# Kernel optimization log

Hardware: AMD Instinct MI355X
Metric: run time of the kernel (lower is better)

## Reference

```python
import jax, jax.numpy as jnp
import numpy as np

N = 50000
E = 1_600_000
IN_C, HID_C, OUT_C = 128, 64, 16
NEG_SLOPE = 0.2


def setup_inputs() -> dict:
    key = jax.random.key(0)
    ks = jax.random.split(key, 16)
    x = jax.random.normal(ks[0], (N, IN_C), dtype=jnp.float32)
    edge_index = jax.random.randint(ks[1], (2, E), 0, N, dtype=jnp.int32)
    edge_weight = jax.random.uniform(ks[2], (E,), dtype=jnp.float32)

    def lin(k, fan_in, fan_out):
        s = (6.0 / (fan_in + fan_out)) ** 0.5
        return jax.random.uniform(k, (fan_in, fan_out), jnp.float32, -s, s)

    params = {
        "W1": lin(ks[3], IN_C, HID_C),
        "a_src1": jax.random.normal(ks[4], (HID_C,), jnp.float32) * 0.1,
        "a_dst1": jax.random.normal(ks[5], (HID_C,), jnp.float32) * 0.1,
        "b1": jnp.zeros((HID_C,), jnp.float32),
        "W2": lin(ks[6], HID_C, HID_C),
        "a_src2": jax.random.normal(ks[7], (HID_C,), jnp.float32) * 0.1,
        "a_dst2": jax.random.normal(ks[8], (HID_C,), jnp.float32) * 0.1,
        "b2": jnp.zeros((HID_C,), jnp.float32),
        "W3": lin(ks[9], HID_C, OUT_C),
        "a_src3": jax.random.normal(ks[10], (OUT_C,), jnp.float32) * 0.1,
        "a_dst3": jax.random.normal(ks[11], (OUT_C,), jnp.float32) * 0.1,
        "b3": jnp.zeros((OUT_C,), jnp.float32),
    }
    return {"x": x, "edge_index": edge_index, "edge_weight": edge_weight, **params}


def gat_conv(x, W, a_src, a_dst, b, src, dst):
    """Single-head PyG GATConv, add_self_loops=False, eval mode."""
    h = x @ W                                    # [N, C]
    alpha_src = (h * a_src).sum(-1)              # [N]
    alpha_dst = (h * a_dst).sum(-1)              # [N]
    e = jax.nn.leaky_relu(alpha_src[src] + alpha_dst[dst], NEG_SLOPE)  # [E]
    # softmax over incoming edges of each target node
    m = jax.ops.segment_max(e, dst, num_segments=N)
    e = jnp.exp(e - m[dst])
    denom = jax.ops.segment_sum(e, dst, num_segments=N)
    alpha = e / (denom[dst] + 1e-16)             # [E]
    out = jax.ops.segment_sum(h[src] * alpha[:, None], dst, num_segments=N)
    return out + b


def reference(x, edge_index, edge_weight,
              W1, a_src1, a_dst1, b1,
              W2, a_src2, a_dst2, b2,
              W3, a_src3, a_dst3, b3):
    src, dst = edge_index[0], edge_index[1]
    # edge_weight unused: GATConv has no lin_edge (edge_dim=None)
    h = jax.nn.relu(gat_conv(x, W1, a_src1, a_dst1, b1, src, dst))
    h = jax.nn.relu(gat_conv(h, W2, a_src2, a_dst2, b2, src, dst))
    return gat_conv(h, W3, a_src3, a_dst3, b3, src, dst)
```

## Files before the change

### kernel.cpp

```cpp
#include <hip/hip_runtime.h>
#include <hip/hip_fp16.h>
#include <math.h>

#define N_NODES 50000
#define N_EDGES 1600000
#define BSH 8
#define NBUCK ((N_NODES + 255) >> BSH)
#define EPB 4096
#define NBLK ((N_EDGES + EPB - 1) / EPB)


__global__ __launch_bounds__(256) void bucket_hist(const int* __restrict__ dst,
                                                   int* __restrict__ bhist_t, int e) {
    __shared__ int h[NBUCK];
    for (int i = threadIdx.x; i < NBUCK; i += 256) h[i] = 0;
    __syncthreads();
    int base = blockIdx.x * EPB;
#pragma unroll
    for (int j = 0; j < EPB / 256; ++j) {
        int i = base + j * 256 + threadIdx.x;
        if (i < e) atomicAdd(&h[dst[i] >> BSH], 1);
    }
    __syncthreads();
    for (int i = threadIdx.x; i < NBUCK; i += 256)
        bhist_t[i * NBLK + blockIdx.x] = h[i];
}

__global__ __launch_bounds__(256) void bucket_totals(const int* __restrict__ bhist_t,
                                                     int* __restrict__ btot) {
    int b = blockIdx.x;
    const int* col = bhist_t + (size_t)b * NBLK;
    int s = 0;
    for (int i = threadIdx.x; i < NBLK; i += 256) s += col[i];
#pragma unroll
    for (int off = 1; off < 64; off <<= 1) s += __shfl_xor(s, off);
    __shared__ int red[4];
    if ((threadIdx.x & 63) == 0) red[threadIdx.x >> 6] = s;
    __syncthreads();
    if (threadIdx.x == 0)
        btot[b] = red[0] + red[1] + red[2] + red[3];
}

__global__ __launch_bounds__(64) void rewrite_offsets(int* __restrict__ bhist_t,
                                                      const int* __restrict__ btot,
                                                      int* __restrict__ rowptr) {
    int b = blockIdx.x;
    int lane = threadIdx.x;
    int pre = 0;
    for (int i = lane; i < NBUCK; i += 64) if (i < b) pre += btot[i];
#pragma unroll
    for (int off = 1; off < 64; off <<= 1) pre += __shfl_xor(pre, off);
    if (b == 0 && lane == 0) rowptr[N_NODES] = N_EDGES;

    int* col = bhist_t + (size_t)b * NBLK;
    __shared__ int buf[NBLK];
    for (int i = lane; i < NBLK; i += 64) buf[i] = col[i];
    __syncthreads();
    constexpr int CH = (NBLK + 63) / 64;
    int lo = lane * CH;
    int hi = lo + CH; if (hi > NBLK) hi = NBLK;
    int s = 0;
    for (int i = lo; i < hi; ++i) s += buf[i];
    int inc = s;
#pragma unroll
    for (int off = 1; off < 64; off <<= 1) {
        int t = __shfl_up(inc, off);
        if (lane >= off) inc += t;
    }
    int run = pre + inc - s;
    for (int i = lo; i < hi; ++i) { int c = buf[i]; col[i] = run; run += c; }
}

__global__ __launch_bounds__(256) void bucket_scatter(const int* __restrict__ src,
                                                      const int* __restrict__ dst,
                                                      const int* __restrict__ bhist_t,
                                                      unsigned* __restrict__ packed, int e) {
    __shared__ int lcur[NBUCK];
    int r = blockIdx.x;
    for (int i = threadIdx.x; i < NBUCK; i += 256)
        lcur[i] = bhist_t[i * NBLK + r];
    __syncthreads();
    int base = r * EPB;
#pragma unroll
    for (int j = 0; j < EPB / 256; ++j) {
        int i = base + j * 256 + threadIdx.x;
        if (i < e) {
            int d = dst[i];
            int pos = atomicAdd(&lcur[d >> BSH], 1);
            packed[pos] = (unsigned)src[i] | ((unsigned)(d & ((1 << BSH) - 1)) << 16);
        }
    }
}

__global__ __launch_bounds__(512) void csr_finalize(const unsigned* __restrict__ packed,
                                                    const int* __restrict__ btot,
                                                    int* __restrict__ rowptr,
                                                    int* __restrict__ csr_src) {
    int b = blockIdx.x;
    __shared__ int sb[2];
    if (threadIdx.x < 64) {
        int pre = 0, tot = 0;
        for (int i = threadIdx.x; i < NBUCK; i += 64) {
            int v = btot[i];
            if (i < b) pre += v;
            if (i == b) tot = v;
        }
#pragma unroll
        for (int off = 1; off < 64; off <<= 1) {
            pre += __shfl_xor(pre, off);
            tot += __shfl_xor(tot, off);
        }
        if (threadIdx.x == 0) { sb[0] = pre; sb[1] = pre + tot; }
    }
    __syncthreads();
    int s0 = sb[0], s1 = sb[1];
    int cnt = s1 - s0;
    __shared__ int ncnt[256];
    __shared__ int ncur[256];
    __shared__ int wsum[4];
    if (threadIdx.x < 256) ncnt[threadIdx.x] = 0;
    __syncthreads();
    for (int i = threadIdx.x; i < cnt; i += 512)
        atomicAdd(&ncnt[packed[s0 + i] >> 16], 1);
    __syncthreads();
    int lane = threadIdx.x & 63, w = threadIdx.x >> 6;
    int v = 0, inc = 0;
    if (threadIdx.x < 256) {
        v = ncnt[threadIdx.x]; inc = v;
#pragma unroll
        for (int off = 1; off < 64; off <<= 1) {
            int t = __shfl_up(inc, off);
            if (lane >= off) inc += t;
        }
        if (lane == 63) wsum[w] = inc;
    }
    __syncthreads();
    if (threadIdx.x < 256) {
        int woff = 0;
#pragma unroll
        for (int k = 0; k < 3; ++k) if (k < w) woff += wsum[k];
        int excl = woff + inc - v;
        int node = (b << BSH) + threadIdx.x;
        if (node < N_NODES) rowptr[node] = s0 + excl;
        ncur[threadIdx.x] = s0 + excl;
    }
    __syncthreads();
    for (int i = threadIdx.x; i < cnt; i += 512) {
        unsigned p = packed[s0 + i];
        int pos = atomicAdd(&ncur[p >> 16], 1);
        csr_src[pos] = (int)(p & 0xFFFFu);
    }
}


template<int K, int C, bool IN_HALF, bool OUT_HALF>
__global__ __launch_bounds__(256) void gemm_alpha(
        const void* __restrict__ inv, const float* __restrict__ W,
        const float* __restrict__ a_src, const float* __restrict__ a_dst,
        void* __restrict__ hv, float* __restrict__ as_, float* __restrict__ ad_, int n)
{
    constexpr int CPT = C / 16;
    constexpr int KP = K + 4;
    __shared__ float sx[64][KP];
    __shared__ float sW[K * C];
    int row0 = blockIdx.x * 64;
    int nvalid = n - row0;

    if constexpr (IN_HALF) {
        const __half* inh = (const __half*)inv;
        for (int idx = threadIdx.x; idx < 64 * K / 8; idx += 256) {
            int r = idx / (K / 8), kc = idx % (K / 8);
            uint4 v = {0u, 0u, 0u, 0u};
            if (r < nvalid) v = *(const uint4*)&inh[(size_t)(row0 + r) * K + kc * 8];
            float2 f0 = __half22float2(*(__half2*)&v.x);
            float2 f1 = __half22float2(*(__half2*)&v.y);
            float2 f2 = __half22float2(*(__half2*)&v.z);
            float2 f3 = __half22float2(*(__half2*)&v.w);
            float* d = &sx[r][kc * 8];
            d[0] = f0.x; d[1] = f0.y; d[2] = f1.x; d[3] = f1.y;
            d[4] = f2.x; d[5] = f2.y; d[6] = f3.x; d[7] = f3.y;
        }
    } else {
        const float* in = (const float*)inv;
        for (int idx = threadIdx.x; idx < 64 * K / 4; idx += 256) {
            int r = idx / (K / 4), kc = idx % (K / 4);
            float4 v = {0, 0, 0, 0};
            if (r < nvalid) v = *(const float4*)&in[(size_t)(row0 + r) * K + kc * 4];
            *(float4*)&sx[r][kc * 4] = v;
        }
    }
    for (int idx = threadIdx.x; idx < K * C / 4; idx += 256)
        *(float4*)&sW[idx * 4] = *(const float4*)&W[idx * 4];
    __syncthreads();

    int g  = threadIdx.x >> 4;
    int ci = threadIdx.x & 15;
    int r0 = g * 4;
    int c0 = ci * CPT;

    if constexpr (CPT == 4) {
        float4 acc0 = {0,0,0,0}, acc1 = {0,0,0,0}, acc2 = {0,0,0,0}, acc3 = {0,0,0,0};
        for (int k = 0; k < K; k += 4) {
            float4 w0 = *(const float4*)&sW[(k + 0) * C + c0];
            float4 w1 = *(const float4*)&sW[(k + 1) * C + c0];
            float4 w2 = *(const float4*)&sW[(k + 2) * C + c0];
            float4 w3 = *(const float4*)&sW[(k + 3) * C + c0];
            float4 x0 = *(const float4*)&sx[r0 + 0][k];
            float4 x1 = *(const float4*)&sx[r0 + 1][k];
            float4 x2 = *(const float4*)&sx[r0 + 2][k];
            float4 x3 = *(const float4*)&sx[r0 + 3][k];
#define STEP(A, X) \
            A.x = fmaf(X.x, w0.x, A.x); A.y = fmaf(X.x, w0.y, A.y); \
            A.z = fmaf(X.x, w0.z, A.z); A.w = fmaf(X.x, w0.w, A.w); \
            A.x = fmaf(X.y, w1.x, A.x); A.y = fmaf(X.y, w1.y, A.y); \
            A.z = fmaf(X.y, w1.z, A.z); A.w = fmaf(X.y, w1.w, A.w); \
            A.x = fmaf(X.z, w2.x, A.x); A.y = fmaf(X.z, w2.y, A.y); \
            A.z = fmaf(X.z, w2.z, A.z); A.w = fmaf(X.z, w2.w, A.w); \
            A.x = fmaf(X.w, w3.x, A.x); A.y = fmaf(X.w, w3.y, A.y); \
            A.z = fmaf(X.w, w3.z, A.z); A.w = fmaf(X.w, w3.w, A.w);
            STEP(acc0, x0) STEP(acc1, x1) STEP(acc2, x2) STEP(acc3, x3)
#undef STEP
        }
        if constexpr (OUT_HALF) {
            __half* hh = (__half*)hv;
            auto sth = [&](int r, float4 a) {
                if (r0 + r < nvalid) {
                    size_t base = (size_t)(row0 + r0 + r) * C + c0;
                    *(__half2*)&hh[base]     = __floats2half2_rn(a.x, a.y);
                    *(__half2*)&hh[base + 2] = __floats2half2_rn(a.z, a.w);
                }
            };
            sth(0, acc0); sth(1, acc1); sth(2, acc2); sth(3, acc3);
        } else {
            float* h = (float*)hv;
            if (r0 + 0 < nvalid) *(float4*)&h[(size_t)(row0 + r0 + 0) * C + c0] = acc0;
            if (r0 + 1 < nvalid) *(float4*)&h[(size_t)(row0 + r0 + 1) * C + c0] = acc1;
            if (r0 + 2 < nvalid) *(float4*)&h[(size_t)(row0 + r0 + 2) * C + c0] = acc2;
            if (r0 + 3 < nvalid) *(float4*)&h[(size_t)(row0 + r0 + 3) * C + c0] = acc3;
        }
        float4 asv = *(const float4*)&a_src[c0];
        float4 adv = *(const float4*)&a_dst[c0];
        float vs0 = acc0.x*asv.x + acc0.y*asv.y + acc0.z*asv.z + acc0.w*asv.w;
        float vs1 = acc1.x*asv.x + acc1.y*asv.y + acc1.z*asv.z + acc1.w*asv.w;
        float vs2 = acc2.x*asv.x + acc2.y*asv.y + acc2.z*asv.z + acc2.w*asv.w;
        float vs3 = acc3.x*asv.x + acc3.y*asv.y + acc3.z*asv.z + acc3.w*asv.w;
        float vd0 = acc0.x*adv.x + acc0.y*adv.y + acc0.z*adv.z + acc0.w*adv.w;
        float vd1 = acc1.x*adv.x + acc1.y*adv.y + acc1.z*adv.z + acc1.w*adv.w;
        float vd2 = acc2.x*adv.x + acc2.y*adv.y + acc2.z*adv.z + acc2.w*adv.w;
        float vd3 = acc3.x*adv.x + acc3.y*adv.y + acc3.z*adv.z + acc3.w*adv.w;
#pragma unroll
        for (int off = 1; off < 16; off <<= 1) {
            vs0 += __shfl_xor(vs0, off); vs1 += __shfl_xor(vs1, off);
            vs2 += __shfl_xor(vs2, off); vs3 += __shfl_xor(vs3, off);
            vd0 += __shfl_xor(vd0, off); vd1 += __shfl_xor(vd1, off);
            vd2 += __shfl_xor(vd2, off); vd3 += __shfl_xor(vd3, off);
        }
        if (ci == 0) {
            if (r0 + 0 < nvalid) { as_[row0+r0+0] = vs0; ad_[row0+r0+0] = vd0; }
            if (r0 + 1 < nvalid) { as_[row0+r0+1] = vs1; ad_[row0+r0+1] = vd1; }
            if (r0 + 2 < nvalid) { as_[row0+r0+2] = vs2; ad_[row0+r0+2] = vd2; }
            if (r0 + 3 < nvalid) { as_[row0+r0+3] = vs3; ad_[row0+r0+3] = vd3; }
        }
    } else {
        float s0 = 0.f, s1 = 0.f, s2 = 0.f, s3 = 0.f;
        for (int k = 0; k < K; k += 4) {
            float w0 = sW[(k + 0) * C + c0];
            float w1 = sW[(k + 1) * C + c0];
            float w2 = sW[(k + 2) * C + c0];
            float w3 = sW[(k + 3) * C + c0];
            float4 x0 = *(const float4*)&sx[r0 + 0][k];
            float4 x1 = *(const float4*)&sx[r0 + 1][k];
            float4 x2 = *(const float4*)&sx[r0 + 2][k];
            float4 x3 = *(const float4*)&sx[r0 + 3][k];
            s0 = fmaf(x0.x,w0, fmaf(x0.y,w1, fmaf(x0.z,w2, fmaf(x0.w,w3, s0))));
            s1 = fmaf(x1.x,w0, fmaf(x1.y,w1, fmaf(x1.z,w2, fmaf(x1.w,w3, s1))));
            s2 = fmaf(x2.x,w0, fmaf(x2.y,w1, fmaf(x2.z,w2, fmaf(x2.w,w3, s2))));
            s3 = fmaf(x3.x,w0, fmaf(x3.y,w1, fmaf(x3.z,w2, fmaf(x3.w,w3, s3))));
        }
        if constexpr (OUT_HALF) {
            __half* hh = (__half*)hv;
            if (r0 + 0 < nvalid) hh[(size_t)(row0+r0+0) * C + c0] = __float2half_rn(s0);
            if (r0 + 1 < nvalid) hh[(size_t)(row0+r0+1) * C + c0] = __float2half_rn(s1);
            if (r0 + 2 < nvalid) hh[(size_t)(row0+r0+2) * C + c0] = __float2half_rn(s2);
            if (r0 + 3 < nvalid) hh[(size_t)(row0+r0+3) * C + c0] = __float2half_rn(s3);
        } else {
            float* h = (float*)hv;
            if (r0 + 0 < nvalid) h[(size_t)(row0+r0+0) * C + c0] = s0;
            if (r0 + 1 < nvalid) h[(size_t)(row0+r0+1) * C + c0] = s1;
            if (r0 + 2 < nvalid) h[(size_t)(row0+r0+2) * C + c0] = s2;
            if (r0 + 3 < nvalid) h[(size_t)(row0+r0+3) * C + c0] = s3;
        }
        float as0 = a_src[c0], ad0 = a_dst[c0];
        float vs0 = s0*as0, vs1 = s1*as0, vs2 = s2*as0, vs3 = s3*as0;
        float vd0 = s0*ad0, vd1 = s1*ad0, vd2 = s2*ad0, vd3 = s3*ad0;
#pragma unroll
        for (int off = 1; off < 16; off <<= 1) {
            vs0 += __shfl_xor(vs0, off); vs1 += __shfl_xor(vs1, off);
            vs2 += __shfl_xor(vs2, off); vs3 += __shfl_xor(vs3, off);
            vd0 += __shfl_xor(vd0, off); vd1 += __shfl_xor(vd1, off);
            vd2 += __shfl_xor(vd2, off); vd3 += __shfl_xor(vd3, off);
        }
        if (ci == 0) {
            if (r0 + 0 < nvalid) { as_[row0+r0+0] = vs0; ad_[row0+r0+0] = vd0; }
            if (r0 + 1 < nvalid) { as_[row0+r0+1] = vs1; ad_[row0+r0+1] = vd1; }
            if (r0 + 2 < nvalid) { as_[row0+r0+2] = vs2; ad_[row0+r0+2] = vd2; }
            if (r0 + 3 < nvalid) { as_[row0+r0+3] = vs3; ad_[row0+r0+3] = vd3; }
        }
    }
}


__device__ __forceinline__ float leaky(float e) {
    return (e >= 0.f) ? e : 0.2f * e;
}

__device__ __forceinline__ void hacc8(uint4 r, float w, float4& accL, float4& accH) {
    float2 f0 = __half22float2(*(__half2*)&r.x);
    float2 f1 = __half22float2(*(__half2*)&r.y);
    float2 f2 = __half22float2(*(__half2*)&r.z);
    float2 f3 = __half22float2(*(__half2*)&r.w);
    accL.x = fmaf(w, f0.x, accL.x); accL.y = fmaf(w, f0.y, accL.y);
    accL.z = fmaf(w, f1.x, accL.z); accL.w = fmaf(w, f1.y, accL.w);
    accH.x = fmaf(w, f2.x, accH.x); accH.y = fmaf(w, f2.y, accH.y);
    accH.z = fmaf(w, f3.x, accH.z); accH.w = fmaf(w, f3.y, accH.w);
}

template<bool RELU>
__global__ __launch_bounds__(256) void agg64h(
        const __half* __restrict__ h, const float* __restrict__ as_, const float* __restrict__ ad_,
        const int* __restrict__ rowptr, const int* __restrict__ csr_src,
        const float* __restrict__ bias, __half* __restrict__ out, int n)
{
    int node = (blockIdx.x * blockDim.x + threadIdx.x) >> 6;
    if (node >= n) return;
    int lane = threadIdx.x & 63;
    int g  = lane >> 3;
    int c8 = lane & 7;
    int start = rowptr[node], end = rowptr[node + 1];
    float adn = ad_[node];
    const char* hb = (const char*)h + (size_t)c8 * 16;

    float4 accL = {0,0,0,0}, accH = {0,0,0,0};
    float dsum = 0.f;

    for (int chunk = start; chunk < end; chunk += 64) {
        int e_i = chunk + lane;
        int soff = 0; float aw = 0.f;
        if (e_i < end) {
            int ssrc = csr_src[e_i];
            soff = ssrc << 7;
            aw = __expf(leaky(as_[ssrc] + adn));
        }
        dsum += aw;
        int nv = end - chunk; if (nv > 64) nv = 64;
        int nvu = (nv + 31) & ~31;
        for (int j = g; j < nvu; j += 32) {
            int   o0 = __shfl(soff, j),      o1 = __shfl(soff, j + 8);
            int   o2 = __shfl(soff, j + 16), o3 = __shfl(soff, j + 24);
            float w0 = __shfl(aw, j),        w1 = __shfl(aw, j + 8);
            float w2 = __shfl(aw, j + 16),   w3 = __shfl(aw, j + 24);
            uint4 r0 = *(const uint4*)(hb + o0);
            uint4 r1 = *(const uint4*)(hb + o1);
            uint4 r2 = *(const uint4*)(hb + o2);
            uint4 r3 = *(const uint4*)(hb + o3);
            hacc8(r0, w0, accL, accH); hacc8(r1, w1, accL, accH);
            hacc8(r2, w2, accL, accH); hacc8(r3, w3, accL, accH);
        }
    }
#pragma unroll
    for (int off = 8; off <= 32; off <<= 1) {
        accL.x += __shfl_xor(accL.x, off); accL.y += __shfl_xor(accL.y, off);
        accL.z += __shfl_xor(accL.z, off); accL.w += __shfl_xor(accL.w, off);
        accH.x += __shfl_xor(accH.x, off); accH.y += __shfl_xor(accH.y, off);
        accH.z += __shfl_xor(accH.z, off); accH.w += __shfl_xor(accH.w, off);
    }
#pragma unroll
    for (int off = 1; off <= 32; off <<= 1) dsum += __shfl_xor(dsum, off);

    if (g == 0) {
        float inv = 1.f / (dsum + 1e-16f);
        float4 bl = *(const float4*)&bias[c8 * 8];
        float4 bh = *(const float4*)&bias[c8 * 8 + 4];
        float4 ol, oh;
        ol.x = fmaf(accL.x, inv, bl.x); ol.y = fmaf(accL.y, inv, bl.y);
        ol.z = fmaf(accL.z, inv, bl.z); ol.w = fmaf(accL.w, inv, bl.w);
        oh.x = fmaf(accH.x, inv, bh.x); oh.y = fmaf(accH.y, inv, bh.y);
        oh.z = fmaf(accH.z, inv, bh.z); oh.w = fmaf(accH.w, inv, bh.w);
        if (RELU) {
            ol.x = fmaxf(ol.x, 0.f); ol.y = fmaxf(ol.y, 0.f);
            ol.z = fmaxf(ol.z, 0.f); ol.w = fmaxf(ol.w, 0.f);
            oh.x = fmaxf(oh.x, 0.f); oh.y = fmaxf(oh.y, 0.f);
            oh.z = fmaxf(oh.z, 0.f); oh.w = fmaxf(oh.w, 0.f);
        }
        __half2 p0 = __floats2half2_rn(ol.x, ol.y);
        __half2 p1 = __floats2half2_rn(ol.z, ol.w);
        __half2 p2 = __floats2half2_rn(oh.x, oh.y);
        __half2 p3 = __floats2half2_rn(oh.z, oh.w);
        uint4 pk;
        pk.x = *(unsigned*)&p0; pk.y = *(unsigned*)&p1;
        pk.z = *(unsigned*)&p2; pk.w = *(unsigned*)&p3;
        *(uint4*)&out[(size_t)node * 64 + c8 * 8] = pk;
    }
}

template<bool RELU>
__global__ __launch_bounds__(256) void agg16h(
        const __half* __restrict__ h, const float* __restrict__ as_, const float* __restrict__ ad_,
        const int* __restrict__ rowptr, const int* __restrict__ csr_src,
        const float* __restrict__ bias, float* __restrict__ out, int n)
{
    int node = (blockIdx.x * blockDim.x + threadIdx.x) >> 6;
    if (node >= n) return;
    int lane = threadIdx.x & 63;
    int g   = lane >> 1;
    int c16 = lane & 1;
    int start = rowptr[node], end = rowptr[node + 1];
    float adn = ad_[node];
    const char* hb = (const char*)h + (size_t)c16 * 16;

    float4 accL = {0,0,0,0}, accH = {0,0,0,0};
    float dsum = 0.f;

    for (int chunk = start; chunk < end; chunk += 64) {
        int e_i = chunk + lane;
        int soff = 0; float aw = 0.f;
        if (e_i < end) {
            int ssrc = csr_src[e_i];
            soff = ssrc << 5;
            aw = __expf(leaky(as_[ssrc] + adn));
        }
        dsum += aw;
        int nv = end - chunk; if (nv > 64) nv = 64;
        int nvu = (nv + 31) & ~31;
        for (int j = g; j < nvu; j += 32) {
            int   o0 = __shfl(soff, j);
            float w0 = __shfl(aw, j);
            uint4 r0 = *(const uint4*)(hb + o0);
            hacc8(r0, w0, accL, accH);
        }
    }
#pragma unroll
    for (int off = 2; off <= 32; off <<= 1) {
        accL.x += __shfl_xor(accL.x, off); accL.y += __shfl_xor(accL.y, off);
        accL.z += __shfl_xor(accL.z, off); accL.w += __shfl_xor(accL.w, off);
        accH.x += __shfl_xor(accH.x, off); accH.y += __shfl_xor(accH.y, off);
        accH.z += __shfl_xor(accH.z, off); accH.w += __shfl_xor(accH.w, off);
    }
#pragma unroll
    for (int off = 1; off <= 32; off <<= 1) dsum += __shfl_xor(dsum, off);

    if (g == 0) {
        float inv = 1.f / (dsum + 1e-16f);
        float4 bl = *(const float4*)&bias[c16 * 8];
        float4 bh = *(const float4*)&bias[c16 * 8 + 4];
        float4 ol, oh;
        ol.x = fmaf(accL.x, inv, bl.x); ol.y = fmaf(accL.y, inv, bl.y);
        ol.z = fmaf(accL.z, inv, bl.z); ol.w = fmaf(accL.w, inv, bl.w);
        oh.x = fmaf(accH.x, inv, bh.x); oh.y = fmaf(accH.y, inv, bh.y);
        oh.z = fmaf(accH.z, inv, bh.z); oh.w = fmaf(accH.w, inv, bh.w);
        if (RELU) {
            ol.x = fmaxf(ol.x, 0.f); ol.y = fmaxf(ol.y, 0.f);
            ol.z = fmaxf(ol.z, 0.f); ol.w = fmaxf(ol.w, 0.f);
            oh.x = fmaxf(oh.x, 0.f); oh.y = fmaxf(oh.y, 0.f);
            oh.z = fmaxf(oh.z, 0.f); oh.w = fmaxf(oh.w, 0.f);
        }
        *(float4*)&out[(size_t)node * 16 + c16 * 8]     = ol;
        *(float4*)&out[(size_t)node * 16 + c16 * 8 + 4] = oh;
    }
}


extern "C" void kernel_launch(void* const* d_in, const int* in_sizes, int n_in,
                              void* d_out, int out_size, void* d_ws, size_t ws_size,
                              hipStream_t stream) {
    const float* x   = (const float*)d_in[0];
    const int*   ei  = (const int*)  d_in[1];
    const float* W1  = (const float*)d_in[3];
    const float* as1 = (const float*)d_in[4];
    const float* ad1 = (const float*)d_in[5];
    const float* b1  = (const float*)d_in[6];
    const float* W2  = (const float*)d_in[7];
    const float* as2 = (const float*)d_in[8];
    const float* ad2 = (const float*)d_in[9];
    const float* b2  = (const float*)d_in[10];
    const float* W3  = (const float*)d_in[11];
    const float* as3 = (const float*)d_in[12];
    const float* ad3 = (const float*)d_in[13];
    const float* b3  = (const float*)d_in[14];

    const int* srcp = ei;
    const int* dstp = ei + N_EDGES;

    char* ws = (char*)d_ws;
    size_t off = 0;
    auto alloc = [&](size_t bytes) -> void* {
        void* p = ws + off;
        off = (off + bytes + 255) & ~(size_t)255;
        return p;
    };
    int*   bhist_t = (int*)   alloc((size_t)NBUCK * NBLK * sizeof(int));
    int*   btot    = (int*)   alloc(NBUCK * sizeof(int));
    int*   rowptr  = (int*)   alloc((N_NODES + 1) * sizeof(int));
    int*   csr_src = (int*)   alloc(N_EDGES * sizeof(int));
    float* asb     = (float*) alloc(N_NODES * sizeof(float));
    float* adb     = (float*) alloc(N_NODES * sizeof(float));
    __half* hHalf  = (__half*)alloc((size_t)N_NODES * 64 * sizeof(__half));
    __half* aHalf  = (__half*)alloc((size_t)N_NODES * 64 * sizeof(__half));
    __half* h16    = (__half*)alloc((size_t)N_NODES * 16 * sizeof(__half));
    unsigned* packed = (unsigned*)alloc((size_t)N_EDGES * sizeof(unsigned));

    bucket_hist    <<<NBLK,  256, 0, stream>>>(dstp, bhist_t, N_EDGES);
    bucket_totals  <<<NBUCK, 256, 0, stream>>>(bhist_t, btot);
    rewrite_offsets<<<NBUCK, 64,  0, stream>>>(bhist_t, btot, rowptr);
    bucket_scatter <<<NBLK,  256, 0, stream>>>(srcp, dstp, bhist_t, packed, N_EDGES);
    csr_finalize   <<<NBUCK, 512, 0, stream>>>(packed, btot, rowptr, csr_src);

    const int NB64 = (N_NODES + 63) / 64;
    const int NB4  = (N_NODES + 3) / 4;

    gemm_alpha<128, 64, false, true><<<NB64, 256, 0, stream>>>(x, W1, as1, ad1, hHalf, asb, adb, N_NODES);
    agg64h<true><<<NB4, 256, 0, stream>>>(hHalf, asb, adb, rowptr, csr_src, b1, aHalf, N_NODES);

    gemm_alpha<64, 64, true, true><<<NB64, 256, 0, stream>>>(aHalf, W2, as2, ad2, hHalf, asb, adb, N_NODES);
    agg64h<true><<<NB4, 256, 0, stream>>>(hHalf, asb, adb, rowptr, csr_src, b2, aHalf, N_NODES);

    gemm_alpha<64, 16, true, true><<<NB64, 256, 0, stream>>>(aHalf, W3, as3, ad3, h16, asb, adb, N_NODES);
    agg16h<false><<<NB4, 256, 0, stream>>>(h16, asb, adb, rowptr, csr_src, b3, (float*)d_out, N_NODES);
}
```

Measured before the change: 189.5 us.

## Stage bucket scatter in LDS for coalesced writes and shrink csr_src to 16-bit

The bucket scatter kernel now ranks each edge within its bucket in shared memory, prefix-sums the per-bucket counts, stages the packed edges sorted by bucket in LDS, and then writes them out in bucket-contiguous runs, so global stores become mostly coalesced instead of scattered. The edges-per-block count is halved to fit the staging buffers and add parallelism, at the cost of a larger histogram. csr_src is stored as unsigned short, halving CSR index traffic in the three aggregation passes. The 16-bit index relies on node ids fitting in 16 bits, which holds for 50000 nodes but assumes that bound.

```diff
diff --git a/kernel.cpp b/kernel.cpp
--- a/kernel.cpp
+++ b/kernel.cpp
@@ -6,7 +6,7 @@
 #define N_EDGES 1600000
 #define BSH 8
 #define NBUCK ((N_NODES + 255) >> BSH)
-#define EPB 4096
+#define EPB 2048
 #define NBLK ((N_EDGES + EPB - 1) / EPB)
 
 
@@ -75,27 +75,71 @@
                                                       const int* __restrict__ dst,
                                                       const int* __restrict__ bhist_t,
                                                       unsigned* __restrict__ packed, int e) {
-    __shared__ int lcur[NBUCK];
+    __shared__ int lcnt[NBUCK];
+    __shared__ int lbase[NBUCK];
+    __shared__ int gbase[NBUCK];
+    __shared__ unsigned stage[EPB];
+    __shared__ unsigned char sbk[EPB];
+    __shared__ int wsum[4];
     int r = blockIdx.x;
-    for (int i = threadIdx.x; i < NBUCK; i += 256)
-        lcur[i] = bhist_t[i * NBLK + r];
+    for (int i = threadIdx.x; i < NBUCK; i += 256) {
+        lcnt[i] = 0;
+        gbase[i] = bhist_t[i * NBLK + r];
+    }
     __syncthreads();
     int base = r * EPB;
+    int bk[EPB / 256], lrank[EPB / 256];
+    unsigned pk[EPB / 256];
+    bool val[EPB / 256];
 #pragma unroll
     for (int j = 0; j < EPB / 256; ++j) {
         int i = base + j * 256 + threadIdx.x;
-        if (i < e) {
+        val[j] = (i < e);
+        if (val[j]) {
             int d = dst[i];
-            int pos = atomicAdd(&lcur[d >> BSH], 1);
-            packed[pos] = (unsigned)src[i] | ((unsigned)(d & ((1 << BSH) - 1)) << 16);
-        }
+            bk[j] = d >> BSH;
+            pk[j] = (unsigned)src[i] | ((unsigned)(d & ((1 << BSH) - 1)) << 16);
+            lrank[j] = atomicAdd(&lcnt[bk[j]], 1);
+        }
+    }
+    __syncthreads();
+    {
+        int lane = threadIdx.x & 63, w = threadIdx.x >> 6;
+        int v = (threadIdx.x < NBUCK) ? lcnt[threadIdx.x] : 0;
+        int inc = v;
+#pragma unroll
+        for (int off = 1; off < 64; off <<= 1) {
+            int t = __shfl_up(inc, off);
+            if (lane >= off) inc += t;
+        }
+        if (lane == 63) wsum[w] = inc;
+        __syncthreads();
+        int woff = 0;
+#pragma unroll
+        for (int k = 0; k < 3; ++k) if (k < w) woff += wsum[k];
+        if (threadIdx.x < NBUCK) lbase[threadIdx.x] = woff + inc - v;
+    }
+    __syncthreads();
+#pragma unroll
+    for (int j = 0; j < EPB / 256; ++j) {
+        if (val[j]) {
+            int slot = lbase[bk[j]] + lrank[j];
+            stage[slot] = pk[j];
+            sbk[slot] = (unsigned char)bk[j];
+        }
+    }
+    __syncthreads();
+    int vn = e - base; if (vn > EPB) vn = EPB;
+    for (int i = threadIdx.x; i < vn; i += 256) {
+        int b = sbk[i];
+        packed[gbase[b] + (i - lbase[b])] = stage[i];
     }
 }
 
 __global__ __launch_bounds__(512) void csr_finalize(const unsigned* __restrict__ packed,
                                                     const int* __restrict__ btot,
                                                     int* __restrict__ rowptr,
-                                                    int* __restrict__ csr_src) {
+                                                    unsigned short* __restrict__ csr_src) {
     int b = blockIdx.x;
     __shared__ int sb[2];
     if (threadIdx.x < 64) {
@@ -148,7 +192,7 @@
     for (int i = threadIdx.x; i < cnt; i += 512) {
         unsigned p = packed[s0 + i];
         int pos = atomicAdd(&ncur[p >> 16], 1);
-        csr_src[pos] = (int)(p & 0xFFFFu);
+        csr_src[pos] = (unsigned short)(p & 0xFFFFu);
     }
 }
 
@@ -328,7 +372,7 @@
 template<bool RELU>
 __global__ __launch_bounds__(256) void agg64h(
         const __half* __restrict__ h, const float* __restrict__ as_, const float* __restrict__ ad_,
-        const int* __restrict__ rowptr, const int* __restrict__ csr_src,
+        const int* __restrict__ rowptr, const unsigned short* __restrict__ csr_src,
         const float* __restrict__ bias, __half* __restrict__ out, int n)
 {
     int node = (blockIdx.x * blockDim.x + threadIdx.x) >> 6;
@@ -406,7 +450,7 @@
 template<bool RELU>
 __global__ __launch_bounds__(256) void agg16h(
         const __half* __restrict__ h, const float* __restrict__ as_, const float* __restrict__ ad_,
-        const int* __restrict__ rowptr, const int* __restrict__ csr_src,
+        const int* __restrict__ rowptr, const unsigned short* __restrict__ csr_src,
         const float* __restrict__ bias, float* __restrict__ out, int n)
 {
     int node = (blockIdx.x * blockDim.x + threadIdx.x) >> 6;
@@ -501,7 +545,7 @@
     int*   bhist_t = (int*)   alloc((size_t)NBUCK * NBLK * sizeof(int));
     int*   btot    = (int*)   alloc(NBUCK * sizeof(int));
     int*   rowptr  = (int*)   alloc((N_NODES + 1) * sizeof(int));
-    int*   csr_src = (int*)   alloc(N_EDGES * sizeof(int));
+    unsigned short* csr_src = (unsigned short*)alloc((size_t)N_EDGES * sizeof(unsigned short));
     float* asb     = (float*) alloc(N_NODES * sizeof(float));
     float* adb     = (float*) alloc(N_NODES * sizeof(float));
     __half* hHalf  = (__half*)alloc((size_t)N_NODES * 64 * sizeof(__half));
```

New measurement: 184.4 us. 1.03x faster.
